# Kernel optimization log

Measured on AMD Instinct MI355X. Metric: run time of the kernel, lower is better.

Reference implementation:

```python
import jax, jax.numpy as jnp
import numpy as np

B, S, T, D = 32, 8, 128, 768   # batch, num_sentences, seq_len, embedding_dim
A, L = 8, 8                    # num_args, arg_length


def _extract(sentence_embeddings, sentence_ids, token_ids):
    """Vectorized form of extract_embeddings_from_ids.

    For each (b, s, a): average, over nonzero token ids l, the embedding at the
    sentence position whose id equals token_ids[b,s,a,l]. token_id == 0 is skipped.
    sentence_ids are unique per sentence, so each id matches exactly one position
    (the only case where the original loop yields shape [B,S,A,D]).
    """
    valid = token_ids != 0                                            # [B,S,A,L]
    # match[b,s,a,l,t] = token matches sentence position t (and token is nonzero)
    match = (token_ids[..., None] == sentence_ids[:, :, None, None, :]) & valid[..., None]
    # gather matched embeddings per token: [B,S,A,L,D]
    gathered = jnp.einsum('bsalt,bstd->bsald', match.astype(sentence_embeddings.dtype),
                          sentence_embeddings)
    n_valid = jnp.maximum(valid.sum(-1), 1).astype(sentence_embeddings.dtype)  # [B,S,A]
    return gathered.sum(axis=3) / n_valid[..., None]                  # [B,S,A,D]


def setup_inputs() -> dict:
    key = jax.random.key(0)
    k_emb, k_p, k_a0, k_a1 = jax.random.split(key, 4)
    sentence_embeddings = jax.random.normal(k_emb, (B, S, T, D), dtype=jnp.float32)
    # unique token ids 1..T per sentence (0 is reserved as padding/skip)
    sentence_ids = jnp.broadcast_to(jnp.arange(1, T + 1, dtype=jnp.int64), (B, S, T))
    predicate_ids = jax.random.randint(k_p, (B, S, A, L), 0, T, dtype=jnp.int64)
    arg0_ids = jax.random.randint(k_a0, (B, S, A, L), 0, T, dtype=jnp.int64)
    arg1_ids = jax.random.randint(k_a1, (B, S, A, L), 0, T, dtype=jnp.int64)
    return {
        'sentence_embeddings': sentence_embeddings,
        'sentence_ids': sentence_ids,
        'predicate_ids': predicate_ids,
        'arg0_ids': arg0_ids,
        'arg1_ids': arg1_ids,
    }


def reference(sentence_embeddings, sentence_ids, predicate_ids, arg0_ids, arg1_ids):
    sentence_average_embeddings = sentence_embeddings.mean(axis=2)     # [B,S,D]
    predicate_embeddings = _extract(sentence_embeddings, sentence_ids, predicate_ids)
    arg0_embeddings = _extract(sentence_embeddings, sentence_ids, arg0_ids)
    arg1_embeddings = _extract(sentence_embeddings, sentence_ids, arg1_ids)
    return (sentence_average_embeddings, predicate_embeddings,
            arg0_embeddings, arg1_embeddings)
```

## Files before the change

### kernel.cpp

```cpp
#include <hip/hip_runtime.h>

namespace {
constexpr int B_ = 32, S_ = 8, T_ = 128, D_ = 768, A_ = 8, L_ = 8;
constexpr int BS = B_ * S_;
constexpr int MEAN_ELEMS = BS * D_;
constexpr int EXT_ELEMS  = BS * A_ * D_;
constexpr int D4 = D_ / 4;
constexpr int MEAN_BLOCKS = BS;
constexpr int EXT_BLOCKS  = BS * A_;

__global__ void __launch_bounds__(256) srl_one(
    const float* __restrict__ emb,
    const int* __restrict__ sids,
    const int* __restrict__ pred,
    const int* __restrict__ arg0,
    const int* __restrict__ arg1,
    float* __restrict__ out)
{
    const int blk = blockIdx.x;
    const int tid = threadIdx.x;

    if (blk < MEAN_BLOCKS) {
        if (tid >= 192) return;
        const int bs = blk;
        const float4* p = reinterpret_cast<const float4*>(emb + (size_t)bs * T_ * D_) + tid;
        float4 acc = {0.f, 0.f, 0.f, 0.f};
        #pragma unroll 8
        for (int t = 0; t < T_; ++t) {
            float4 v = p[(size_t)t * D4];
            acc.x += v.x; acc.y += v.y; acc.z += v.z; acc.w += v.w;
        }
        const float s = 1.0f / T_;
        float4 r = {acc.x * s, acc.y * s, acc.z * s, acc.w * s};
        reinterpret_cast<float4*>(out)[(size_t)bs * D4 + tid] = r;
        return;
    }

    const int eblk = blk - MEAN_BLOCKS;
    const int bs = eblk >> 3, a = eblk & 7;
    constexpr int NT = 3 * L_;
    __shared__ int toks[NT];
    __shared__ int pos[NT];
    __shared__ float invs[3];

    if (tid < NT) {
        int e = tid >> 3, l = tid & 7;
        const int* p = (e == 0) ? pred : ((e == 1) ? arg0 : arg1);
        toks[tid] = p[(size_t)(bs * A_ + a) * L_ + l];
        pos[tid] = -1;
    }
    __syncthreads();
    if (tid < T_) {
        int id = sids[(size_t)bs * T_ + tid];
        #pragma unroll
        for (int i = 0; i < NT; ++i)
            if (toks[i] != 0 && toks[i] == id) pos[i] = tid;
    } else if (tid >= 128 && tid < 128 + 3) {
        int e = tid - 128, n = 0;
        #pragma unroll
        for (int l = 0; l < L_; ++l) n += (toks[e * L_ + l] != 0);
        invs[e] = 1.0f / (float)(n < 1 ? 1 : n);
    }
    __syncthreads();

    const float* base = emb + (size_t)bs * T_ * D_;
    float acc[3][3] = {};
    #pragma unroll
    for (int e = 0; e < 3; ++e) {
        #pragma unroll
        for (int l = 0; l < L_; ++l) {
            int p = pos[e * L_ + l];
            if (p >= 0) {
                const float* row = base + (size_t)p * D_;
                acc[e][0] += row[tid];
                acc[e][1] += row[tid + 256];
                acc[e][2] += row[tid + 512];
            }
        }
    }
    #pragma unroll
    for (int e = 0; e < 3; ++e) {
        float iv = invs[e];
        float* o = out + MEAN_ELEMS + (size_t)e * EXT_ELEMS + (size_t)(bs * A_ + a) * D_;
        o[tid]       = acc[e][0] * iv;
        o[tid + 256] = acc[e][1] * iv;
        o[tid + 512] = acc[e][2] * iv;
    }
}
}

extern "C" void kernel_launch(void* const* d_in, const int* in_sizes, int n_in,
                              void* d_out, int out_size, void* d_ws, size_t ws_size,
                              hipStream_t stream) {
    const float* emb  = (const float*)d_in[0];
    const int*   sids = (const int*)d_in[1];
    const int*   pred = (const int*)d_in[2];
    const int*   arg0 = (const int*)d_in[3];
    const int*   arg1 = (const int*)d_in[4];
    float* out = (float*)d_out;

    srl_one<<<dim3(MEAN_BLOCKS + EXT_BLOCKS), dim3(256), 0, stream>>>(
        emb, sids, pred, arg0, arg1, out);
}
```

Before: 43.85 us.

## Split sequence mean over T chunks with workspace partials and reduce kernel

The mean over the sequence axis now runs as 8 chunk blocks per sentence, which write partial sums to workspace, and a second kernel reduces them. Previously one long-running block per sentence did all of it. This spreads the 25MB streaming read over more blocks to cut tail latency. The extraction path now uses 192 threads with float4 loads and branchless weighted accumulation. A fallback keeps the old single kernel when the workspace is too small. The cost is a second launch and a workspace round trip.

```diff
diff --git a/kernel.cpp b/kernel.cpp
--- a/kernel.cpp
+++ b/kernel.cpp
@@ -6,10 +6,106 @@
 constexpr int MEAN_ELEMS = BS * D_;
 constexpr int EXT_ELEMS  = BS * A_ * D_;
 constexpr int D4 = D_ / 4;
-constexpr int MEAN_BLOCKS = BS;
+constexpr int TSPLIT = 8, TCH = T_ / TSPLIT;
+constexpr int PART_BLOCKS = BS * TSPLIT;
 constexpr int EXT_BLOCKS  = BS * A_;
-
-__global__ void __launch_bounds__(256) srl_one(
+constexpr int NTHR = 192;
+constexpr size_t WS_FLOATS = (size_t)TSPLIT * BS * D_;
+
+__global__ void __launch_bounds__(NTHR) srl_main(
+    const float* __restrict__ emb,
+    const int* __restrict__ sids,
+    const int* __restrict__ pred,
+    const int* __restrict__ arg0,
+    const int* __restrict__ arg1,
+    float* __restrict__ ws,
+    float* __restrict__ out)
+{
+    const int blk = blockIdx.x;
+    const int tid = threadIdx.x;
+
+    if (blk < PART_BLOCKS) {
+        int bs = blk >> 3, ch = blk & 7;
+        const float4* p = reinterpret_cast<const float4*>(emb + (size_t)bs * T_ * D_)
+                          + (size_t)(ch * TCH) * D4 + tid;
+        float4 acc = {0.f, 0.f, 0.f, 0.f};
+        #pragma unroll
+        for (int t = 0; t < TCH; ++t) {
+            float4 v = p[(size_t)t * D4];
+            acc.x += v.x; acc.y += v.y; acc.z += v.z; acc.w += v.w;
+        }
+        reinterpret_cast<float4*>(ws)[(size_t)blk * D4 + tid] = acc;
+        return;
+    }
+
+    const int eblk = blk - PART_BLOCKS;
+    const int bs = eblk >> 3, a = eblk & 7;
+    constexpr int NT = 3 * L_;
+    __shared__ int toks[NT];
+    __shared__ int pos[NT];
+    __shared__ float invs[3];
+
+    if (tid < NT) {
+        int e = tid >> 3, l = tid & 7;
+        const int* p = (e == 0) ? pred : ((e == 1) ? arg0 : arg1);
+        toks[tid] = p[(size_t)(bs * A_ + a) * L_ + l];
+        pos[tid] = -1;
+    }
+    __syncthreads();
+    if (tid < T_) {
+        int id = sids[(size_t)bs * T_ + tid];
+        #pragma unroll
+        for (int i = 0; i < NT; ++i)
+            if (toks[i] != 0 && toks[i] == id) pos[i] = tid;
+    } else if (tid >= 128 && tid < 131) {
+        int e = tid - 128, n = 0;
+        #pragma unroll
+        for (int l = 0; l < L_; ++l) n += (toks[e * L_ + l] != 0);
+        invs[e] = 1.0f / (float)(n < 1 ? 1 : n);
+    }
+    __syncthreads();
+
+    const float4* base4 = reinterpret_cast<const float4*>(emb + (size_t)bs * T_ * D_);
+    float4 acc[3] = {};
+    #pragma unroll
+    for (int e = 0; e < 3; ++e) {
+        #pragma unroll
+        for (int l = 0; l < L_; ++l) {
+            int p = pos[e * L_ + l];
+            float w = (p >= 0) ? 1.0f : 0.0f;
+            int pr = (p >= 0) ? p : 0;
+            float4 v = base4[(size_t)pr * D4 + tid];
+            acc[e].x += w * v.x; acc[e].y += w * v.y;
+            acc[e].z += w * v.z; acc[e].w += w * v.w;
+        }
+    }
+    #pragma unroll
+    for (int e = 0; e < 3; ++e) {
+        float iv = invs[e];
+        float4 r = {acc[e].x * iv, acc[e].y * iv, acc[e].z * iv, acc[e].w * iv};
+        reinterpret_cast<float4*>(out + MEAN_ELEMS + (size_t)e * EXT_ELEMS
+                                  + (size_t)(bs * A_ + a) * D_)[tid] = r;
+    }
+}
+
+__global__ void __launch_bounds__(256) srl_reduce(
+    const float* __restrict__ ws, float* __restrict__ out)
+{
+    int idx = blockIdx.x * 256 + threadIdx.x;
+    int bs = idx / D4, d4 = idx % D4;
+    const float4* w = reinterpret_cast<const float4*>(ws);
+    float4 acc = {0.f, 0.f, 0.f, 0.f};
+    #pragma unroll
+    for (int ch = 0; ch < TSPLIT; ++ch) {
+        float4 v = w[(size_t)(bs * TSPLIT + ch) * D4 + d4];
+        acc.x += v.x; acc.y += v.y; acc.z += v.z; acc.w += v.w;
+    }
+    const float s = 1.0f / T_;
+    float4 r = {acc.x * s, acc.y * s, acc.z * s, acc.w * s};
+    reinterpret_cast<float4*>(out)[idx] = r;
+}
+
+__global__ void __launch_bounds__(256) srl_fallback(
     const float* __restrict__ emb,
     const int* __restrict__ sids,
     const int* __restrict__ pred,
@@ -19,11 +115,9 @@
 {
     const int blk = blockIdx.x;
     const int tid = threadIdx.x;
-
-    if (blk < MEAN_BLOCKS) {
+    if (blk < BS) {
         if (tid >= 192) return;
-        const int bs = blk;
-        const float4* p = reinterpret_cast<const float4*>(emb + (size_t)bs * T_ * D_) + tid;
+        const float4* p = reinterpret_cast<const float4*>(emb + (size_t)blk * T_ * D_) + tid;
         float4 acc = {0.f, 0.f, 0.f, 0.f};
         #pragma unroll 8
         for (int t = 0; t < T_; ++t) {
@@ -32,17 +126,15 @@
         }
         const float s = 1.0f / T_;
         float4 r = {acc.x * s, acc.y * s, acc.z * s, acc.w * s};
-        reinterpret_cast<float4*>(out)[(size_t)bs * D4 + tid] = r;
+        reinterpret_cast<float4*>(out)[(size_t)blk * D4 + tid] = r;
         return;
     }
-
-    const int eblk = blk - MEAN_BLOCKS;
+    const int eblk = blk - BS;
     const int bs = eblk >> 3, a = eblk & 7;
     constexpr int NT = 3 * L_;
     __shared__ int toks[NT];
     __shared__ int pos[NT];
     __shared__ float invs[3];
-
     if (tid < NT) {
         int e = tid >> 3, l = tid & 7;
         const int* p = (e == 0) ? pred : ((e == 1) ? arg0 : arg1);
@@ -55,36 +147,34 @@
         #pragma unroll
         for (int i = 0; i < NT; ++i)
             if (toks[i] != 0 && toks[i] == id) pos[i] = tid;
-    } else if (tid >= 128 && tid < 128 + 3) {
+    } else if (tid >= 128 && tid < 131) {
         int e = tid - 128, n = 0;
         #pragma unroll
         for (int l = 0; l < L_; ++l) n += (toks[e * L_ + l] != 0);
         invs[e] = 1.0f / (float)(n < 1 ? 1 : n);
     }
     __syncthreads();
-
-    const float* base = emb + (size_t)bs * T_ * D_;
-    float acc[3][3] = {};
+    if (tid >= 192) return;
+    const float4* base4 = reinterpret_cast<const float4*>(emb + (size_t)bs * T_ * D_);
+    float4 acc[3] = {};
     #pragma unroll
     for (int e = 0; e < 3; ++e) {
         #pragma unroll
         for (int l = 0; l < L_; ++l) {
             int p = pos[e * L_ + l];
-            if (p >= 0) {
-                const float* row = base + (size_t)p * D_;
-                acc[e][0] += row[tid];
-                acc[e][1] += row[tid + 256];
-                acc[e][2] += row[tid + 512];
-            }
+            float w = (p >= 0) ? 1.0f : 0.0f;
+            int pr = (p >= 0) ? p : 0;
+            float4 v = base4[(size_t)pr * D4 + tid];
+            acc[e].x += w * v.x; acc[e].y += w * v.y;
+            acc[e].z += w * v.z; acc[e].w += w * v.w;
         }
     }
     #pragma unroll
     for (int e = 0; e < 3; ++e) {
         float iv = invs[e];
-        float* o = out + MEAN_ELEMS + (size_t)e * EXT_ELEMS + (size_t)(bs * A_ + a) * D_;
-        o[tid]       = acc[e][0] * iv;
-        o[tid + 256] = acc[e][1] * iv;
-        o[tid + 512] = acc[e][2] * iv;
+        float4 r = {acc[e].x * iv, acc[e].y * iv, acc[e].z * iv, acc[e].w * iv};
+        reinterpret_cast<float4*>(out + MEAN_ELEMS + (size_t)e * EXT_ELEMS
+                                  + (size_t)(bs * A_ + a) * D_)[tid] = r;
     }
 }
 }
@@ -98,7 +188,14 @@
     const int*   arg0 = (const int*)d_in[3];
     const int*   arg1 = (const int*)d_in[4];
     float* out = (float*)d_out;
-
-    srl_one<<<dim3(MEAN_BLOCKS + EXT_BLOCKS), dim3(256), 0, stream>>>(
-        emb, sids, pred, arg0, arg1, out);
-}
+    float* ws  = (float*)d_ws;
+
+    if (ws_size >= WS_FLOATS * sizeof(float)) {
+        srl_main<<<dim3(PART_BLOCKS + EXT_BLOCKS), dim3(NTHR), 0, stream>>>(
+            emb, sids, pred, arg0, arg1, ws, out);
+        srl_reduce<<<dim3(BS * D4 / 256), dim3(256), 0, stream>>>(ws, out);
+    } else {
+        srl_fallback<<<dim3(BS + EXT_BLOCKS), dim3(256), 0, stream>>>(
+            emb, sids, pred, arg0, arg1, out);
+    }
+}
```

After: 45.84 us. 1.05x slower.
